# Kernel optimization log

Measured on AMD Instinct MI355X. Metric: run time of the kernel, lower is better.

## Reference

```python
import jax, jax.numpy as jnp
import numpy as np

B = 1024          # number of sessions (graphs)
D = 128           # emb_dim
NH = 4            # num_heads
VOCAB = 50000     # POI vocabulary
NDIST = 512       # distance buckets
MAX_LEN = 160     # max session length


def _lengths():
    # deterministic variable session lengths in [64, 160]
    return np.asarray(64 + (np.arange(B) % 97), dtype=np.int64)


def _layernorm(x, g, b, eps=1e-8):
    mu = x.mean(-1, keepdims=True)
    var = ((x - mu) ** 2).mean(-1, keepdims=True)
    return (x - mu) / jnp.sqrt(var + eps) * g + b


def setup_inputs() -> dict:
    key = jax.random.key(0)
    ks = jax.random.split(key, 16)
    lengths = _lengths()
    N = int(lengths.sum())
    # node -> (graph id, position within graph)
    batch_ids = np.repeat(np.arange(B), lengths)
    node_pos = np.concatenate([np.arange(l) for l in lengths])
    # consecutive (sequence) edges within each session
    starts = np.concatenate([[0], np.cumsum(lengths)[:-1]])
    src = np.concatenate([s + np.arange(l - 1) for s, l in zip(starts, lengths)])
    dst = src + 1
    edge_index = np.stack([src, dst]).astype(np.int64)
    E = edge_index.shape[1]
    s = 1.0 / np.sqrt(D)
    return {
        "POI_embs": jax.random.normal(ks[0], (VOCAB, D), jnp.float32) * 0.02,
        "delta_dis_embs": jax.random.normal(ks[1], (NDIST, D), jnp.float32) * 0.02,
        "att_W": jax.random.normal(ks[2], (D, D), jnp.float32) * s,
        "a_src": jax.random.normal(ks[3], (D,), jnp.float32) * 0.1,
        "a_dst": jax.random.normal(ks[4], (D,), jnp.float32) * 0.1,
        "in_proj_w": jax.random.normal(ks[5], (3 * D, D), jnp.float32) * s,
        "in_proj_b": jnp.zeros((3 * D,), jnp.float32),
        "out_proj_w": jax.random.normal(ks[6], (D, D), jnp.float32) * s,
        "out_proj_b": jnp.zeros((D,), jnp.float32),
        "ln1_g": jnp.ones((D,), jnp.float32), "ln1_b": jnp.zeros((D,), jnp.float32),
        "ln2_g": jnp.ones((D,), jnp.float32), "ln2_b": jnp.zeros((D,), jnp.float32),
        "ffn_w1": jax.random.normal(ks[7], (D, D), jnp.float32) * s,
        "ffn_b1": jnp.zeros((D,), jnp.float32),
        "ffn_w2": jax.random.normal(ks[8], (D, D), jnp.float32) * s,
        "ffn_b2": jnp.zeros((D,), jnp.float32),
        "sess_idx": jax.random.randint(ks[9], (N,), 0, VOCAB),
        "edge_dist": jax.random.randint(ks[10], (E,), 0, NDIST),
        "edge_index": jnp.asarray(edge_index),
        "batch_ids": jnp.asarray(batch_ids),
        "node_pos": jnp.asarray(node_pos),
        "lengths": jnp.asarray(lengths),
    }


def reference(POI_embs, delta_dis_embs, att_W, a_src, a_dst,
              in_proj_w, in_proj_b, out_proj_w, out_proj_b,
              ln1_g, ln1_b, ln2_g, ln2_b,
              ffn_w1, ffn_b1, ffn_w2, ffn_b2,
              sess_idx, edge_dist, edge_index, batch_ids, node_pos, lengths):
    N = sess_idx.shape[0]
    E = edge_index.shape[1]
    # ---- BiSeqGCN: gather -> attention logits -> scatter-softmax -> scatter-add
    x = POI_embs[sess_idx]                    # [N, D] node features
    edge_l = delta_dis_embs[edge_dist]        # [E, D] edge features
    src, dst = edge_index[0], edge_index[1]
    # bidirectional edges: forward (src->dst) then reversed (dst->src)
    j = jnp.concatenate([src, dst])           # message source  x_j
    i = jnp.concatenate([dst, src])           # message target  x_i
    x_i = x[i]                                # [2E, D]
    x_j = x[j]                                # [2E, D]
    fwd_coeff = (x_i[:E] + edge_l) @ att_W.T  # [E, D]
    bwd_coeff = x_i[E:] @ att_W.T             # [E, D]
    logits = jnp.concatenate([fwd_coeff @ a_src, bwd_coeff @ a_dst])  # [2E]
    # scatter-softmax over destination node (torch_geometric softmax, eps=1e-16)
    m = jax.ops.segment_max(logits, i, num_segments=N)
    e = jnp.exp(logits - m[i])
    ssum = jax.ops.segment_sum(e, i, num_segments=N)
    attn = e / (ssum[i] + 1e-16)
    H_u = jax.ops.segment_sum(x_j * attn[:, None], i, num_segments=N)  # [N, D]
    # ---- split/pad to [B, Lmax, D] + padding mask
    Bn = lengths.shape[0]
    pad = jnp.zeros((Bn, MAX_LEN, D), H_u.dtype).at[batch_ids, node_pos].set(H_u)
    mask = jnp.arange(MAX_LEN)[None, :] < lengths[:, None]  # [B, Lmax]
    # ---- MultiheadAttention (Q = LayerNorm(pad); K = V = pad)
    Q = _layernorm(pad, ln1_g, ln1_b)
    Wq, Wk, Wv = jnp.split(in_proj_w, 3, axis=0)
    bq, bk, bv = jnp.split(in_proj_b, 3)
    hd = D // NH
    q = (Q @ Wq.T + bq).reshape(Bn, MAX_LEN, NH, hd)
    k = (pad @ Wk.T + bk).reshape(Bn, MAX_LEN, NH, hd)
    v = (pad @ Wv.T + bv).reshape(Bn, MAX_LEN, NH, hd)
    scores = jnp.einsum('bqhd,bkhd->bhqk', q, k) / jnp.sqrt(jnp.asarray(hd, q.dtype))
    scores = jnp.where(mask[:, None, None, :], scores, -jnp.inf)
    w = jax.nn.softmax(scores, axis=-1)
    ctx = jnp.einsum('bhqk,bkhd->bqhd', w, v).reshape(Bn, MAX_LEN, D)
    out = ctx @ out_proj_w.T + out_proj_b
    out = out + Q
    out = _layernorm(out, ln2_g, ln2_b)
    # ---- PFFN (1x1 convs == per-token linears) with residual
    ffn = jax.nn.relu(out @ ffn_w1.T + ffn_b1) @ ffn_w2.T + ffn_b2
    out = out + ffn
    # ---- masked mean pool over valid positions
    mf = mask[..., None].astype(out.dtype)
    S_u = (out * mf).sum(axis=1) / lengths[:, None].astype(out.dtype)
    return S_u
```

## Files before the change

### kernel.cpp

```cpp
#include <hip/hip_runtime.h>
#include <float.h>


#define D 128
#define NHEAD 4
#define HD 32
#define MAXL 160
#define MAXNK 10
#define VP 168
#define WP 136

typedef __attribute__((ext_vector_type(8))) short short8;
typedef __attribute__((ext_vector_type(4))) float floatx4;

__device__ __forceinline__ float lo2f(unsigned u) {
    union { unsigned i; float f; } x; x.i = u << 16; return x.f;
}
__device__ __forceinline__ float hi2f(unsigned u) {
    union { unsigned i; float f; } x; x.i = u & 0xffff0000u; return x.f;
}
__device__ __forceinline__ unsigned pack2(float a, float b) {
    unsigned r;
    asm("v_cvt_pk_bf16_f32 %0, %1, %2" : "=v"(r) : "v"(a), "v"(b));
    return r;
}
__device__ __forceinline__ unsigned short f2bf(float f) {
    return (unsigned short)pack2(f, 0.f);
}
__device__ __forceinline__ unsigned short f2bfi(float f) {
    union { float f; unsigned i; } x; x.f = f;
    unsigned r = x.i + 0x7fffu + ((x.i >> 16) & 1u);
    return (unsigned short)(r >> 16);
}
__device__ __forceinline__ unsigned pack2i(float a, float b) {
    return (unsigned)f2bfi(a) | ((unsigned)f2bfi(b) << 16);
}
__device__ __forceinline__ float bf2f(unsigned short u) {
    union { unsigned i; float f; } x; x.i = (unsigned)u << 16; return x.f;
}

__launch_bounds__(128)
__global__ void prep1(const float* __restrict__ att_W, const float* __restrict__ a_src,
                      const float* __restrict__ a_dst, const float* __restrict__ in_proj_w,
                      const float* __restrict__ in_proj_b, const float* __restrict__ g1,
                      const float* __restrict__ b1, float* __restrict__ c_src,
                      float* __restrict__ c_dst, float* __restrict__ u, float* __restrict__ z) {
    int p = blockIdx.x;
    int q = threadIdx.x;
    __shared__ float red[4][2];
    float w  = att_W[q * D + p];
    float wq = in_proj_w[p * D + q];
    float s  = a_src[q] * w;
    float d  = a_dst[q] * w;
    float su = g1[q] * wq;
    float sz = b1[q] * wq;
    #pragma unroll
    for (int o = 32; o; o >>= 1) {
        s  += __shfl_down(s, o, 64);
        d  += __shfl_down(d, o, 64);
        su += __shfl_down(su, o, 64);
        sz += __shfl_down(sz, o, 64);
    }
    int wv = q >> 6;
    if ((q & 63) == 0) { red[0][wv] = s; red[1][wv] = d; red[2][wv] = su; red[3][wv] = sz; }
    __syncthreads();
    if (q == 0) {
        c_src[p] = red[0][0] + red[0][1];
        c_dst[p] = red[1][0] + red[1][1];
        u[p]     = red[2][0] + red[2][1];
        z[p]     = red[3][0] + red[3][1] + in_proj_b[p];
    }
}

__global__ void prep2(const float* __restrict__ delta, const float* __restrict__ c_src,
                      const float* __restrict__ in_proj_w, const float* __restrict__ out_proj_w,
                      const float* __restrict__ ffn_w1, const float* __restrict__ ffn_w2,
                      const float* __restrict__ ln1_g, float* __restrict__ tb,
                      unsigned short* __restrict__ wb) {
    int blk = blockIdx.x, t = threadIdx.x;
    if (blk < 128) {
        int b = blk * 4 + (t >> 6);
        int l = t & 63;
        const float* row = delta + (size_t)b * D;
        float s = row[l] * c_src[l] + row[l + 64] * c_src[l + 64];
        #pragma unroll
        for (int o = 32; o; o >>= 1) s += __shfl_down(s, o, 64);
        if (l == 0) tb[b] = s;
    } else {
        int idx = (blk - 128) * 256 + t;
        int m = idx >> 14;
        int within = idx & (D * D - 1);
        float v;
        if (m == 0) v = in_proj_w[within] * ln1_g[within & (D - 1)];
        else if (m == 1) v = in_proj_w[D * D + within];
        else if (m == 2) v = in_proj_w[2 * D * D + within];
        else if (m == 3) v = out_proj_w[within];
        else if (m == 4) v = ffn_w1[within];
        else v = ffn_w2[within];
        wb[idx] = f2bf(v);
    }
}

__launch_bounds__(256)
__global__ void gather_hu(const float* __restrict__ POI, const int* __restrict__ sess_idx,
                          const int* __restrict__ node_pos, const int* __restrict__ batch_ids,
                          const int* __restrict__ edge_dist, const int* __restrict__ lengths,
                          const float* __restrict__ c_src, const float* __restrict__ c_dst,
                          const float* __restrict__ tb, unsigned short* __restrict__ Hu,
                          float* __restrict__ muv, float* __restrict__ rinvv,
                          int* __restrict__ starts, int N) {
    __shared__ unsigned xs[10 * 64];
    __shared__ float s1s[10], s2s[10];
    int R0 = blockIdx.x * 8;
    int t = threadIdx.x;
    int hw = t >> 5, l32 = t & 31;
    float4 cs4 = *(const float4*)(c_src + l32 * 4);
    float4 cd4 = *(const float4*)(c_dst + l32 * 4);
    #pragma unroll
    for (int i = hw; i < 10; i += 8) {
        int n = R0 - 1 + i;
        if (n >= 0 && n < N) {
            int row = sess_idx[n];
            float4 v = *(const float4*)(POI + (size_t)row * D + l32 * 4);
            ((uint2*)(xs + i * 64))[l32] = make_uint2(pack2(v.x, v.y), pack2(v.z, v.w));
            if (i >= 1 && i <= 8) {
                float ps = v.x * cs4.x + v.y * cs4.y + v.z * cs4.z + v.w * cs4.w;
                float pd = v.x * cd4.x + v.y * cd4.y + v.z * cd4.z + v.w * cd4.w;
                #pragma unroll
                for (int o = 16; o; o >>= 1) {
                    ps += __shfl_down(ps, o, 64);
                    pd += __shfl_down(pd, o, 64);
                }
                if (l32 == 0) { s1s[i] = ps; s2s[i] = pd; }
            }
        }
    }
    __syncthreads();
    int j = hw;
    int n = R0 + j;
    if (n >= N) return;
    int g = batch_ids[n], pos = node_pos[n], L = lengths[g];
    bool hasF = pos > 0;
    bool hasB = pos < L - 1;
    float la = hasF ? (s1s[j + 1] + tb[edge_dist[n - 1 - g]]) : -FLT_MAX;
    float lb = hasB ? s2s[j + 1] : -FLT_MAX;
    float m = fmaxf(la, lb);
    float ea = hasF ? __expf(la - m) : 0.f;
    float eb = hasB ? __expf(lb - m) : 0.f;
    float inv = 1.f / (ea + eb + 1e-16f);
    float wa = ea * inv, wb = eb * inv;
    uint2 a = hasF ? ((const uint2*)(xs + j * 64))[l32] : make_uint2(0u, 0u);
    uint2 b = hasB ? ((const uint2*)(xs + (j + 2) * 64))[l32] : make_uint2(0u, 0u);
    float h0 = wa * lo2f(a.x) + wb * lo2f(b.x);
    float h1 = wa * hi2f(a.x) + wb * hi2f(b.x);
    float h2 = wa * lo2f(a.y) + wb * lo2f(b.y);
    float h3 = wa * hi2f(a.y) + wb * hi2f(b.y);
    ((uint2*)Hu)[(size_t)n * 32 + l32] = make_uint2(pack2(h0, h1), pack2(h2, h3));
    float s = h0 + h1 + h2 + h3;
    float ss = h0 * h0 + h1 * h1 + h2 * h2 + h3 * h3;
    #pragma unroll
    for (int o = 1; o < 32; o <<= 1) {
        s += __shfl_xor(s, o, 64);
        ss += __shfl_xor(ss, o, 64);
    }
    if (l32 == 0) {
        float mu = s * (1.f / D);
        float var = ss * (1.f / D) - mu * mu;
        muv[n] = mu;
        rinvv[n] = rsqrtf(var + 1e-8f);
        if (pos == 0) starts[g] = n;
    }
}

__launch_bounds__(256)
__global__ void qkv_split(const unsigned short* __restrict__ Hu, const unsigned short* __restrict__ wb,
                          const float* __restrict__ in_proj_b, const float* __restrict__ u,
                          const float* __restrict__ z, const float* __restrict__ muv,
                          const float* __restrict__ rinvv,
                          unsigned short* __restrict__ qo, unsigned short* __restrict__ ko,
                          unsigned short* __restrict__ vT, int M, int Npad) {
    __shared__ unsigned short Wl[128 * WP];
    int t = threadIdx.x;
    int wv = t >> 6, lane = t & 63;
    int quad = lane >> 4, l16 = lane & 15;
    int r0 = blockIdx.x * 128;
    int rbase = r0 + wv * 32;
    int p = blockIdx.y;
    const float ASCALE = 0.25504364148122793f;
    const unsigned short* W = wb + (p == 0 ? 1 : p == 1 ? 2 : 0) * (D * D);
    for (int i = t; i < 2048; i += 256) {
        int c = i >> 4, kc = (i & 15) * 8;
        *(uint4*)&Wl[c * WP + kc] = *(const uint4*)(W + c * 128 + kc);
    }
    short8 af[2][4];
    #pragma unroll
    for (int mt = 0; mt < 2; mt++) {
        int r = rbase + mt * 16 + l16;
        #pragma unroll
        for (int kk = 0; kk < 4; kk++) {
            if (r < M) af[mt][kk] = *(const short8*)(Hu + (size_t)r * D + kk * 32 + quad * 8);
            else af[mt][kk] = (short8){0, 0, 0, 0, 0, 0, 0, 0};
        }
    }
    __syncthreads();
    floatx4 acc[2][8];
    #pragma unroll
    for (int i = 0; i < 2; i++)
        #pragma unroll
        for (int j = 0; j < 8; j++) acc[i][j] = (floatx4){0.f, 0.f, 0.f, 0.f};
    #pragma unroll
    for (int kk = 0; kk < 4; kk++)
        #pragma unroll
        for (int nt = 0; nt < 8; nt++) {
            short8 bf = *(const short8*)&Wl[(nt * 16 + l16) * WP + kk * 32 + quad * 8];
            acc[0][nt] = __builtin_amdgcn_mfma_f32_16x16x32_bf16(af[0][kk], bf, acc[0][nt], 0, 0, 0);
            acc[1][nt] = __builtin_amdgcn_mfma_f32_16x16x32_bf16(af[1][kk], bf, acc[1][nt], 0, 0, 0);
        }
    __syncthreads();
    if (p == 1) {
        #pragma unroll
        for (int nt = 0; nt < 8; nt++) {
            int col = nt * 16 + l16;
            float bv = in_proj_b[2 * D + col];
            #pragma unroll
            for (int mt = 0; mt < 2; mt++)
                #pragma unroll
                for (int r = 0; r < 4; r += 2) {
                    int ln = wv * 32 + mt * 16 + quad * 4 + r;
                    float v0 = (r0 + ln     < M) ? acc[mt][nt][r]     + bv : 0.f;
                    float v1 = (r0 + ln + 1 < M) ? acc[mt][nt][r + 1] + bv : 0.f;
                    *(unsigned*)&Wl[col * WP + ln] = pack2(v0, v1);
                }
        }
    } else if (p == 0) {
        #pragma unroll
        for (int nt = 0; nt < 8; nt++) {
            int col = nt * 16 + l16;
            float bv = in_proj_b[D + col];
            #pragma unroll
            for (int mt = 0; mt < 2; mt++)
                #pragma unroll
                for (int r = 0; r < 4; r++)
                    Wl[(wv * 32 + mt * 16 + quad * 4 + r) * WP + col] =
                        f2bf(acc[mt][nt][r] + bv);
        }
    } else {
        float uc[8], zc[8];
        #pragma unroll
        for (int nt = 0; nt < 8; nt++) {
            uc[nt] = u[nt * 16 + l16];
            zc[nt] = z[nt * 16 + l16] * ASCALE;
        }
        #pragma unroll
        for (int mt = 0; mt < 2; mt++)
            #pragma unroll
            for (int r = 0; r < 4; r++) {
                int ln = wv * 32 + mt * 16 + quad * 4 + r;
                int grow = r0 + ln;
                float mr = grow < M ? muv[grow] : 0.f;
                float rr = (grow < M ? rinvv[grow] : 0.f) * ASCALE;
                #pragma unroll
                for (int nt = 0; nt < 8; nt++)
                    Wl[ln * WP + nt * 16 + l16] =
                        f2bf(rr * (acc[mt][nt][r] - mr * uc[nt]) + zc[nt]);
            }
    }
    __syncthreads();
    if (p == 1) {
        for (int i = t; i < 2048; i += 256) {
            int col = i >> 4, c8 = (i & 15) * 8;
            *(uint4*)(vT + (size_t)col * Npad + r0 + c8) = *(uint4*)&Wl[col * WP + c8];
        }
    } else {
        unsigned short* out = (p == 0) ? ko : qo;
        for (int i = t; i < 2048; i += 256) {
            int row = i >> 4, c8 = (i & 15) * 8;
            if (r0 + row < M)
                *(uint4*)(out + (size_t)(r0 + row) * D + c8) = *(uint4*)&Wl[row * WP + c8];
        }
    }
}

__launch_bounds__(128)
__global__ void attn9(const unsigned short* __restrict__ qb,
                      const unsigned short* __restrict__ kb,
                      const unsigned short* __restrict__ vT,
                      const int* __restrict__ starts, const int* __restrict__ lengths,
                      unsigned short* __restrict__ ctx, int Npad) {
    __shared__ unsigned short Vt[HD * VP];
    __shared__ unsigned short Pb[2 * 16 * VP];
    int g = blockIdx.x;
    if (gridDim.x == 1024) {
        int bid = blockIdx.x;
        if (bid < 430) { int r = 96 - bid / 10; g = r + 97 * (bid % 10); }
        else { int b2 = bid - 430; int r = 53 - b2 / 11; g = r + 97 * (b2 % 11); }
    }
    int h = blockIdx.y;
    int start = starts[g], L = lengths[g];
    int t = threadIdx.x;
    int wv = t >> 6, lane = t & 63;
    int l16 = lane & 15, quad = lane >> 4;
    int nk = (L + 15) >> 4;
    int nk2 = (L + 31) >> 5;
    unsigned short* Pw = Pb + wv * 16 * VP;
    if (nk & 1) {
        for (int i = lane; i < 128; i += 64) {
            int row = i >> 3, c = i & 7;
            ((unsigned*)(Pw + row * VP + nk * 16))[c] = 0u;
        }
    }
    int nch = nk2 * 4;
    for (int i = t; i < HD * nch; i += 128) {
        int r = i / nch, c = i - r * nch;
        *(uint4*)&Vt[r * VP + c * 8] =
            *(const uint4*)(vT + (size_t)(h * HD + r) * Npad + start + c * 8);
    }
    short8 kf[MAXNK];
    #pragma unroll
    for (int kt = 0; kt < MAXNK; kt++) {
        kf[kt] = (short8){0, 0, 0, 0, 0, 0, 0, 0};
        if (kt < nk) {
            int r = kt * 16 + l16;
            if (r < L) kf[kt] = *(const short8*)(kb + (size_t)(start + r) * D + h * HD + quad * 8);
        }
    }
    short8 qf[5];
    #pragma unroll
    for (int i = 0; i < 5; i++) {
        qf[i] = (short8){0, 0, 0, 0, 0, 0, 0, 0};
        int qt = wv + 2 * i;
        if (qt < nk) {
            int qrow = qt * 16 + l16;
            if (qrow < L)
                qf[i] = *(const short8*)(qb + (size_t)(start + qrow) * D + h * HD + quad * 8);
        }
    }
    __syncthreads();
    #pragma unroll
    for (int i = 0; i < 5; i++) {
        int qt = wv + 2 * i;
        if (qt >= nk) break;
        int q0 = qt * 16;
        floatx4 sacc[MAXNK];
        #pragma unroll
        for (int kt = 0; kt < MAXNK; kt++)
            if (kt < nk)
                sacc[kt] = __builtin_amdgcn_mfma_f32_16x16x32_bf16(
                    kf[kt], qf[i], (floatx4){0.f, 0.f, 0.f, 0.f}, 0, 0, 0);
        float lsum = 0.f;
        #pragma unroll
        for (int kt = 0; kt < MAXNK; kt++)
            if (kt < nk) {
                #pragma unroll
                for (int r = 0; r < 4; r++) {
                    int key = kt * 16 + quad * 4 + r;
                    float p = (key < L) ? __builtin_amdgcn_exp2f(sacc[kt][r]) : 0.f;
                    sacc[kt][r] = p;
                    lsum += p;
                }
                *(uint2*)&Pw[l16 * VP + kt * 16 + quad * 4] =
                    make_uint2(pack2i(sacc[kt][0], sacc[kt][1]),
                               pack2i(sacc[kt][2], sacc[kt][3]));
            }
        lsum += __shfl_xor(lsum, 16);
        lsum += __shfl_xor(lsum, 32);
        float inv = 1.f / lsum;
        #pragma unroll
        for (int nc = 0; nc < 2; nc++) {
            floatx4 oa = (floatx4){0.f, 0.f, 0.f, 0.f};
            floatx4 ob = (floatx4){0.f, 0.f, 0.f, 0.f};
            #pragma unroll
            for (int kc = 0; kc < 5; kc++)
                if (kc < nk2) {
                    short8 pf = *(const short8*)&Pw[l16 * VP + kc * 32 + quad * 8];
                    short8 vf = *(const short8*)&Vt[(nc * 16 + l16) * VP + kc * 32 + quad * 8];
                    if (kc & 1) ob = __builtin_amdgcn_mfma_f32_16x16x32_bf16(pf, vf, ob, 0, 0, 0);
                    else        oa = __builtin_amdgcn_mfma_f32_16x16x32_bf16(pf, vf, oa, 0, 0, 0);
                }
            #pragma unroll
            for (int r = 0; r < 4; r++) {
                int qr = q0 + quad * 4 + r;
                if (qr < L)
                    ctx[(size_t)(start + qr) * D + h * HD + nc * 16 + l16] =
                        f2bfi((oa[r] + ob[r]) * inv);
            }
        }
    }
}

__launch_bounds__(256)
__global__ void outproj_ln2(const unsigned short* __restrict__ ctx, const unsigned short* __restrict__ W,
                            const float* __restrict__ bo, const unsigned short* __restrict__ Hu,
                            const float* __restrict__ muv, const float* __restrict__ rinvv,
                            const float* __restrict__ g1, const float* __restrict__ b1,
                            const float* __restrict__ g2, const float* __restrict__ b2,
                            unsigned short* __restrict__ out, int M) {
    __shared__ unsigned short Wl[128 * WP];
    int t = threadIdx.x;
    int wv = t >> 6, lane = t & 63;
    int quad = lane >> 4, l16 = lane & 15;
    int r0 = blockIdx.x * 128;
    int rbase = r0 + wv * 32;
    for (int i = t; i < 2048; i += 256) {
        int c = i >> 4, kc = (i & 15) * 8;
        *(uint4*)&Wl[c * WP + kc] = *(const uint4*)(W + c * 128 + kc);
    }
    __syncthreads();
    floatx4 acc[2][8];
    #pragma unroll
    for (int i = 0; i < 2; i++)
        #pragma unroll
        for (int j = 0; j < 8; j++) acc[i][j] = (floatx4){0.f, 0.f, 0.f, 0.f};
    #pragma unroll
    for (int kk = 0; kk < 4; kk++) {
        short8 af[2];
        #pragma unroll
        for (int mt = 0; mt < 2; mt++) {
            int r = rbase + mt * 16 + l16;
            if (r < M) af[mt] = *(const short8*)(ctx + (size_t)r * D + kk * 32 + quad * 8);
            else af[mt] = (short8){0, 0, 0, 0, 0, 0, 0, 0};
        }
        #pragma unroll
        for (int nt = 0; nt < 8; nt++) {
            short8 bf = *(const short8*)&Wl[(nt * 16 + l16) * WP + kk * 32 + quad * 8];
            acc[0][nt] = __builtin_amdgcn_mfma_f32_16x16x32_bf16(af[0], bf, acc[0][nt], 0, 0, 0);
            acc[1][nt] = __builtin_amdgcn_mfma_f32_16x16x32_bf16(af[1], bf, acc[1][nt], 0, 0, 0);
        }
    }
    __syncthreads();
    for (int i = t; i < 2048; i += 256) {
        int row = i >> 4, c8 = (i & 15) * 8;
        uint4 hv = make_uint4(0u, 0u, 0u, 0u);
        if (r0 + row < M) hv = *(const uint4*)(Hu + (size_t)(r0 + row) * D + c8);
        *(uint4*)&Wl[row * WP + c8] = hv;
    }
    __syncthreads();
    float g1c[8], b1c[8], boc[8], g2c[8], b2c[8];
    #pragma unroll
    for (int nt = 0; nt < 8; nt++) {
        int col = nt * 16 + l16;
        g1c[nt] = g1[col]; b1c[nt] = b1[col]; boc[nt] = bo[col];
        g2c[nt] = g2[col]; b2c[nt] = b2[col];
    }
    #pragma unroll
    for (int mt = 0; mt < 2; mt++) {
        #pragma unroll
        for (int r = 0; r < 4; r++) {
            int lrow = wv * 32 + mt * 16 + quad * 4 + r;
            int grow = r0 + lrow;
            bool ok = grow < M;
            float mr = ok ? muv[grow] : 0.f;
            float rr = ok ? rinvv[grow] : 0.f;
            float vv[8];
            float s = 0.f, ss = 0.f;
            #pragma unroll
            for (int nt = 0; nt < 8; nt++) {
                float huv = bf2f(Wl[lrow * WP + nt * 16 + l16]);
                float qv = (huv - mr) * rr * g1c[nt] + b1c[nt];
                float v = acc[mt][nt][r] + boc[nt] + qv;
                vv[nt] = v;
                s += v; ss += v * v;
            }
            #pragma unroll
            for (int o = 1; o < 16; o <<= 1) {
                s += __shfl_xor(s, o, 64);
                ss += __shfl_xor(ss, o, 64);
            }
            float mu = s * (1.f / D);
            float var = ss * (1.f / D) - mu * mu;
            float rinv = rsqrtf(var + 1e-8f);
            #pragma unroll
            for (int nt = 0; nt < 8; nt++)
                Wl[lrow * WP + nt * 16 + l16] =
                    f2bf((vv[nt] - mu) * rinv * g2c[nt] + b2c[nt]);
        }
    }
    __syncthreads();
    for (int i = t; i < 2048; i += 256) {
        int row = i >> 4, c8 = (i & 15) * 8;
        if (r0 + row < M)
            *(uint4*)(out + (size_t)(r0 + row) * D + c8) = *(uint4*)&Wl[row * WP + c8];
    }
}

__launch_bounds__(256)
__global__ void ffn_fused(const unsigned short* __restrict__ out2, const unsigned short* __restrict__ W1,
                          const float* __restrict__ b1f, const unsigned short* __restrict__ W2,
                          const float* __restrict__ b2f, unsigned short* __restrict__ fin, int M) {
    __shared__ unsigned short Wl[128 * WP];
    int t = threadIdx.x;
    int wv = t >> 6, lane = t & 63;
    int quad = lane >> 4, l16 = lane & 15;
    int r0 = blockIdx.x * 128;
    int rbase = r0 + wv * 32;
    int lbase = wv * 32;
    for (int i = t; i < 2048; i += 256) {
        int c = i >> 4, kc = (i & 15) * 8;
        *(uint4*)&Wl[c * WP + kc] = *(const uint4*)(W1 + c * 128 + kc);
    }
    short8 af[2][4];
    #pragma unroll
    for (int mt = 0; mt < 2; mt++) {
        int r = rbase + mt * 16 + l16;
        #pragma unroll
        for (int kk = 0; kk < 4; kk++) {
            if (r < M) af[mt][kk] = *(const short8*)(out2 + (size_t)r * D + kk * 32 + quad * 8);
            else af[mt][kk] = (short8){0, 0, 0, 0, 0, 0, 0, 0};
        }
    }
    __syncthreads();
    floatx4 acc[2][8];
    #pragma unroll
    for (int i = 0; i < 2; i++)
        #pragma unroll
        for (int j = 0; j < 8; j++) acc[i][j] = (floatx4){0.f, 0.f, 0.f, 0.f};
    #pragma unroll
    for (int kk = 0; kk < 4; kk++)
        #pragma unroll
        for (int nt = 0; nt < 8; nt++) {
            short8 bf = *(const short8*)&Wl[(nt * 16 + l16) * WP + kk * 32 + quad * 8];
            acc[0][nt] = __builtin_amdgcn_mfma_f32_16x16x32_bf16(af[0][kk], bf, acc[0][nt], 0, 0, 0);
            acc[1][nt] = __builtin_amdgcn_mfma_f32_16x16x32_bf16(af[1][kk], bf, acc[1][nt], 0, 0, 0);
        }
    __syncthreads();
    #pragma unroll
    for (int nt = 0; nt < 8; nt++) {
        int col = nt * 16 + l16;
        float bv = b1f[col];
        #pragma unroll
        for (int mt = 0; mt < 2; mt++)
            #pragma unroll
            for (int r = 0; r < 4; r++)
                Wl[(lbase + mt * 16 + quad * 4 + r) * WP + col] =
                    f2bf(fmaxf(acc[mt][nt][r] + bv, 0.f));
    }
    __syncthreads();
    short8 af2[2][4];
    #pragma unroll
    for (int mt = 0; mt < 2; mt++)
        #pragma unroll
        for (int kk = 0; kk < 4; kk++)
            af2[mt][kk] = *(const short8*)&Wl[(lbase + mt * 16 + l16) * WP + kk * 32 + quad * 8];
    __syncthreads();
    for (int i = t; i < 2048; i += 256) {
        int c = i >> 4, kc = (i & 15) * 8;
        *(uint4*)&Wl[c * WP + kc] = *(const uint4*)(W2 + c * 128 + kc);
    }
    __syncthreads();
    #pragma unroll
    for (int i = 0; i < 2; i++)
        #pragma unroll
        for (int j = 0; j < 8; j++) acc[i][j] = (floatx4){0.f, 0.f, 0.f, 0.f};
    #pragma unroll
    for (int kk = 0; kk < 4; kk++)
        #pragma unroll
        for (int nt = 0; nt < 8; nt++) {
            short8 bf = *(const short8*)&Wl[(nt * 16 + l16) * WP + kk * 32 + quad * 8];
            acc[0][nt] = __builtin_amdgcn_mfma_f32_16x16x32_bf16(af2[0][kk], bf, acc[0][nt], 0, 0, 0);
            acc[1][nt] = __builtin_amdgcn_mfma_f32_16x16x32_bf16(af2[1][kk], bf, acc[1][nt], 0, 0, 0);
        }
    __syncthreads();
    #pragma unroll
    for (int nt = 0; nt < 8; nt++) {
        int col = nt * 16 + l16;
        float bv = b2f[col];
        #pragma unroll
        for (int mt = 0; mt < 2; mt++)
            #pragma unroll
            for (int r = 0; r < 4; r++)
                Wl[(lbase + mt * 16 + quad * 4 + r) * WP + col] = f2bf(acc[mt][nt][r] + bv);
    }
    __syncthreads();
    for (int i = t; i < 2048; i += 256) {
        int row = i >> 4, c8 = (i & 15) * 8;
        int grow = r0 + row;
        if (grow < M) {
            uint4 a = *(uint4*)&Wl[row * WP + c8];
            uint4 b = *(const uint4*)(out2 + (size_t)grow * D + c8);
            uint4 o;
            o.x = pack2(lo2f(a.x) + lo2f(b.x), hi2f(a.x) + hi2f(b.x));
            o.y = pack2(lo2f(a.y) + lo2f(b.y), hi2f(a.y) + hi2f(b.y));
            o.z = pack2(lo2f(a.z) + lo2f(b.z), hi2f(a.z) + hi2f(b.z));
            o.w = pack2(lo2f(a.w) + lo2f(b.w), hi2f(a.w) + hi2f(b.w));
            *(uint4*)(fin + (size_t)grow * D + c8) = o;
        }
    }
}

__launch_bounds__(512)
__global__ void pool_k(const unsigned short* __restrict__ fin, const int* __restrict__ starts,
                       const int* __restrict__ lengths, float* __restrict__ out) {
    __shared__ float ps[4][128];
    int g = blockIdx.x;
    int t = threadIdx.x;
    int d = t & 127, qt = t >> 7;
    int start = starts[g], L = lengths[g];
    int qlen = (L + 3) >> 2;
    int p0 = qt * qlen;
    int p1 = min(L, p0 + qlen);
    float s0 = 0.f, s1 = 0.f, s2 = 0.f, s3 = 0.f;
    int p = p0;
    for (; p + 4 <= p1; p += 4) {
        s0 += bf2f(fin[(size_t)(start + p) * D + d]);
        s1 += bf2f(fin[(size_t)(start + p + 1) * D + d]);
        s2 += bf2f(fin[(size_t)(start + p + 2) * D + d]);
        s3 += bf2f(fin[(size_t)(start + p + 3) * D + d]);
    }
    for (; p < p1; p++) s0 += bf2f(fin[(size_t)(start + p) * D + d]);
    ps[qt][d] = (s0 + s1) + (s2 + s3);
    __syncthreads();
    if (qt == 0)
        out[(size_t)g * D + d] =
            ((ps[0][d] + ps[1][d]) + (ps[2][d] + ps[3][d])) / (float)L;
}

extern "C" void kernel_launch(void* const* d_in, const int* in_sizes, int n_in,
                              void* d_out, int out_size, void* d_ws, size_t ws_size,
                              hipStream_t stream) {
    const float* POI        = (const float*)d_in[0];
    const float* delta      = (const float*)d_in[1];
    const float* att_W      = (const float*)d_in[2];
    const float* a_src      = (const float*)d_in[3];
    const float* a_dst      = (const float*)d_in[4];
    const float* in_proj_w  = (const float*)d_in[5];
    const float* in_proj_b  = (const float*)d_in[6];
    const float* out_proj_w = (const float*)d_in[7];
    const float* out_proj_b = (const float*)d_in[8];
    const float* ln1_g      = (const float*)d_in[9];
    const float* ln1_b      = (const float*)d_in[10];
    const float* ln2_g      = (const float*)d_in[11];
    const float* ln2_b      = (const float*)d_in[12];
    const float* ffn_w1     = (const float*)d_in[13];
    const float* ffn_b1     = (const float*)d_in[14];
    const float* ffn_w2     = (const float*)d_in[15];
    const float* ffn_b2     = (const float*)d_in[16];
    const int* sess_idx     = (const int*)d_in[17];
    const int* edge_dist    = (const int*)d_in[18];
    const int* batch_ids    = (const int*)d_in[20];
    const int* node_pos     = (const int*)d_in[21];
    const int* lengths      = (const int*)d_in[22];

    int N = in_sizes[17];
    int B = in_sizes[22];
    int gb = (N + 127) / 128;
    int Npad = gb * 128;

    char* base = (char*)d_ws;
    size_t off = 0;
    auto alloc = [&](size_t bytes) { size_t c = off; off = (off + bytes + 255) & ~(size_t)255; return c; };
    size_t o_csrc  = alloc(D * 4);
    size_t o_cdst  = alloc(D * 4);
    size_t o_t     = alloc(512 * 4);
    size_t o_start = alloc((size_t)B * 4);
    size_t o_mu    = alloc((size_t)N * 4);
    size_t o_ri    = alloc((size_t)N * 4);
    size_t o_u     = alloc(D * 4);
    size_t o_z     = alloc(D * 4);
    size_t o_wb    = alloc(6 * D * D * 2);
    size_t nb      = (size_t)Npad * D * 2;
    size_t o_A = alloc(nb);
    size_t o_B = alloc(nb);
    size_t o_C = alloc(nb);
    size_t o_D = alloc(nb);
    if (ws_size < off) return;

    float* c_src = (float*)(base + o_csrc);
    float* c_dst = (float*)(base + o_cdst);
    float* tb    = (float*)(base + o_t);
    int*   starts = (int*)(base + o_start);
    float* muv   = (float*)(base + o_mu);
    float* rinvv = (float*)(base + o_ri);
    float* u     = (float*)(base + o_u);
    float* z     = (float*)(base + o_z);
    unsigned short* wb = (unsigned short*)(base + o_wb);
    unsigned short* bufA = (unsigned short*)(base + o_A);
    unsigned short* bufB = (unsigned short*)(base + o_B);
    unsigned short* bufC = (unsigned short*)(base + o_C);
    unsigned short* bufD = (unsigned short*)(base + o_D);

    prep1<<<128, 128, 0, stream>>>(att_W, a_src, a_dst, in_proj_w, in_proj_b,
                                   ln1_g, ln1_b, c_src, c_dst, u, z);
    prep2<<<512, 256, 0, stream>>>(delta, c_src, in_proj_w, out_proj_w,
                                   ffn_w1, ffn_w2, ln1_g, tb, wb);
    gather_hu<<<(N + 7) / 8, 256, 0, stream>>>(POI, sess_idx, node_pos, batch_ids,
                                               edge_dist, lengths, c_src, c_dst, tb,
                                               bufB, muv, rinvv, starts, N);

    qkv_split<<<dim3(gb, 3), 256, 0, stream>>>(bufB, wb, in_proj_b, u, z, muv, rinvv,
                                               bufC, bufD, bufA, N, Npad);

    attn9<<<dim3(B, NHEAD), 128, 0, stream>>>(bufC, bufD, bufA, starts, lengths, bufC, Npad);

    outproj_ln2<<<gb, 256, 0, stream>>>(bufC, wb + 3 * D * D, out_proj_b, bufB, muv, rinvv,
                                        ln1_g, ln1_b, ln2_g, ln2_b, bufD, N);
    ffn_fused<<<gb, 256, 0, stream>>>(bufD, wb + 4 * D * D, ffn_b1, wb + 5 * D * D, ffn_b2,
                                      bufA, N);
    pool_k<<<B, 512, 0, stream>>>(bufA, starts, lengths, (float*)d_out);
}
```

Baseline: 301.1 us.

## Fuse Q/K/V projections into one kernel and double-buffer attention P tiles

The QKV projection no longer launches three grid slices, one per projection. Each block now loads its activation fragments once and runs the K, V and Q GEMMs in sequence, reloading the weight tile into shared memory between them. This cuts activation reloads and block count, but the projections now run serially inside a block, which lowers parallelism and adds barriers. The attention kernel also gives each wave two P buffers, alternating per query tile, so writes for the next tile do not conflict with reads of the previous one. That doubles the shared memory for P.

```diff
diff --git a/kernel.cpp b/kernel.cpp
--- a/kernel.cpp
+++ b/kernel.cpp
@@ -173,7 +173,7 @@
 }
 
 __launch_bounds__(256)
-__global__ void qkv_split(const unsigned short* __restrict__ Hu, const unsigned short* __restrict__ wb,
+__global__ void qkv_fused(const unsigned short* __restrict__ Hu, const unsigned short* __restrict__ wb,
                           const float* __restrict__ in_proj_b, const float* __restrict__ u,
                           const float* __restrict__ z, const float* __restrict__ muv,
                           const float* __restrict__ rinvv,
@@ -185,13 +185,8 @@
     int quad = lane >> 4, l16 = lane & 15;
     int r0 = blockIdx.x * 128;
     int rbase = r0 + wv * 32;
-    int p = blockIdx.y;
     const float ASCALE = 0.25504364148122793f;
-    const unsigned short* W = wb + (p == 0 ? 1 : p == 1 ? 2 : 0) * (D * D);
-    for (int i = t; i < 2048; i += 256) {
-        int c = i >> 4, kc = (i & 15) * 8;
-        *(uint4*)&Wl[c * WP + kc] = *(const uint4*)(W + c * 128 + kc);
-    }
+
     short8 af[2][4];
     #pragma unroll
     for (int mt = 0; mt < 2; mt++) {
@@ -202,8 +197,13 @@
             else af[mt][kk] = (short8){0, 0, 0, 0, 0, 0, 0, 0};
         }
     }
-    __syncthreads();
     floatx4 acc[2][8];
+
+    for (int i = t; i < 2048; i += 256) {
+        int c = i >> 4, kc = (i & 15) * 8;
+        *(uint4*)&Wl[c * WP + kc] = *(const uint4*)(wb + 1 * D * D + c * 128 + kc);
+    }
+    __syncthreads();
     #pragma unroll
     for (int i = 0; i < 2; i++)
         #pragma unroll
@@ -217,34 +217,83 @@
             acc[1][nt] = __builtin_amdgcn_mfma_f32_16x16x32_bf16(af[1][kk], bf, acc[1][nt], 0, 0, 0);
         }
     __syncthreads();
-    if (p == 1) {
+    #pragma unroll
+    for (int nt = 0; nt < 8; nt++) {
+        int col = nt * 16 + l16;
+        float bv = in_proj_b[D + col];
+        #pragma unroll
+        for (int mt = 0; mt < 2; mt++)
+            #pragma unroll
+            for (int r = 0; r < 4; r++)
+                Wl[(wv * 32 + mt * 16 + quad * 4 + r) * WP + col] =
+                    f2bf(acc[mt][nt][r] + bv);
+    }
+    __syncthreads();
+    for (int i = t; i < 2048; i += 256) {
+        int row = i >> 4, c8 = (i & 15) * 8;
+        if (r0 + row < M)
+            *(uint4*)(ko + (size_t)(r0 + row) * D + c8) = *(uint4*)&Wl[row * WP + c8];
+    }
+    __syncthreads();
+
+    for (int i = t; i < 2048; i += 256) {
+        int c = i >> 4, kc = (i & 15) * 8;
+        *(uint4*)&Wl[c * WP + kc] = *(const uint4*)(wb + 2 * D * D + c * 128 + kc);
+    }
+    __syncthreads();
+    #pragma unroll
+    for (int i = 0; i < 2; i++)
+        #pragma unroll
+        for (int j = 0; j < 8; j++) acc[i][j] = (floatx4){0.f, 0.f, 0.f, 0.f};
+    #pragma unroll
+    for (int kk = 0; kk < 4; kk++)
         #pragma unroll
         for (int nt = 0; nt < 8; nt++) {
-            int col = nt * 16 + l16;
-            float bv = in_proj_b[2 * D + col];
-            #pragma unroll
-            for (int mt = 0; mt < 2; mt++)
-                #pragma unroll
-                for (int r = 0; r < 4; r += 2) {
-                    int ln = wv * 32 + mt * 16 + quad * 4 + r;
-                    float v0 = (r0 + ln     < M) ? acc[mt][nt][r]     + bv : 0.f;
-                    float v1 = (r0 + ln + 1 < M) ? acc[mt][nt][r + 1] + bv : 0.f;
-                    *(unsigned*)&Wl[col * WP + ln] = pack2(v0, v1);
-                }
-        }
-    } else if (p == 0) {
+            short8 bf = *(const short8*)&Wl[(nt * 16 + l16) * WP + kk * 32 + quad * 8];
+            acc[0][nt] = __builtin_amdgcn_mfma_f32_16x16x32_bf16(af[0][kk], bf, acc[0][nt], 0, 0, 0);
+            acc[1][nt] = __builtin_amdgcn_mfma_f32_16x16x32_bf16(af[1][kk], bf, acc[1][nt], 0, 0, 0);
+        }
+    __syncthreads();
+    #pragma unroll
+    for (int nt = 0; nt < 8; nt++) {
+        int col = nt * 16 + l16;
+        float bv = in_proj_b[2 * D + col];
+        #pragma unroll
+        for (int mt = 0; mt < 2; mt++)
+            #pragma unroll
+            for (int r = 0; r < 4; r += 2) {
+                int ln = wv * 32 + mt * 16 + quad * 4 + r;
+                float v0 = (r0 + ln     < M) ? acc[mt][nt][r]     + bv : 0.f;
+                float v1 = (r0 + ln + 1 < M) ? acc[mt][nt][r + 1] + bv : 0.f;
+                *(unsigned*)&Wl[col * WP + ln] = pack2(v0, v1);
+            }
+    }
+    __syncthreads();
+    for (int i = t; i < 2048; i += 256) {
+        int col = i >> 4, c8 = (i & 15) * 8;
+        *(uint4*)(vT + (size_t)col * Npad + r0 + c8) = *(uint4*)&Wl[col * WP + c8];
+    }
+    __syncthreads();
+
+    for (int i = t; i < 2048; i += 256) {
+        int c = i >> 4, kc = (i & 15) * 8;
+        *(uint4*)&Wl[c * WP + kc] = *(const uint4*)(wb + 0 * D * D + c * 128 + kc);
+    }
+    __syncthreads();
+    #pragma unroll
+    for (int i = 0; i < 2; i++)
+        #pragma unroll
+        for (int j = 0; j < 8; j++) acc[i][j] = (floatx4){0.f, 0.f, 0.f, 0.f};
+    #pragma unroll
+    for (int kk = 0; kk < 4; kk++)
         #pragma unroll
         for (int nt = 0; nt < 8; nt++) {
-            int col = nt * 16 + l16;
-            float bv = in_proj_b[D + col];
-            #pragma unroll
-            for (int mt = 0; mt < 2; mt++)
-                #pragma unroll
-                for (int r = 0; r < 4; r++)
-                    Wl[(wv * 32 + mt * 16 + quad * 4 + r) * WP + col] =
-                        f2bf(acc[mt][nt][r] + bv);
-        }
-    } else {
+            short8 bf = *(const short8*)&Wl[(nt * 16 + l16) * WP + kk * 32 + quad * 8];
+            acc[0][nt] = __builtin_amdgcn_mfma_f32_16x16x32_bf16(af[0][kk], bf, acc[0][nt], 0, 0, 0);
+            acc[1][nt] = __builtin_amdgcn_mfma_f32_16x16x32_bf16(af[1][kk], bf, acc[1][nt], 0, 0, 0);
+        }
+    __syncthreads();
+    {
         float uc[8], zc[8];
         #pragma unroll
         for (int nt = 0; nt < 8; nt++) {
@@ -266,18 +315,10 @@
             }
     }
     __syncthreads();
-    if (p == 1) {
-        for (int i = t; i < 2048; i += 256) {
-            int col = i >> 4, c8 = (i & 15) * 8;
-            *(uint4*)(vT + (size_t)col * Npad + r0 + c8) = *(uint4*)&Wl[col * WP + c8];
-        }
-    } else {
-        unsigned short* out = (p == 0) ? ko : qo;
-        for (int i = t; i < 2048; i += 256) {
-            int row = i >> 4, c8 = (i & 15) * 8;
-            if (r0 + row < M)
-                *(uint4*)(out + (size_t)(r0 + row) * D + c8) = *(uint4*)&Wl[row * WP + c8];
-        }
+    for (int i = t; i < 2048; i += 256) {
+        int row = i >> 4, c8 = (i & 15) * 8;
+        if (r0 + row < M)
+            *(uint4*)(qo + (size_t)(r0 + row) * D + c8) = *(uint4*)&Wl[row * WP + c8];
     }
 }
 
@@ -288,7 +329,7 @@
                       const int* __restrict__ starts, const int* __restrict__ lengths,
                       unsigned short* __restrict__ ctx, int Npad) {
     __shared__ unsigned short Vt[HD * VP];
-    __shared__ unsigned short Pb[2 * 16 * VP];
+    __shared__ unsigned short Pb[4 * 16 * VP];
     int g = blockIdx.x;
     if (gridDim.x == 1024) {
         int bid = blockIdx.x;
@@ -302,11 +343,12 @@
     int l16 = lane & 15, quad = lane >> 4;
     int nk = (L + 15) >> 4;
     int nk2 = (L + 31) >> 5;
-    unsigned short* Pw = Pb + wv * 16 * VP;
     if (nk & 1) {
-        for (int i = lane; i < 128; i += 64) {
-            int row = i >> 3, c = i & 7;
-            ((unsigned*)(Pw + row * VP + nk * 16))[c] = 0u;
+        for (int i = lane; i < 256; i += 64) {
+            int buf = i >> 7;
+            int j = i & 127;
+            int row = j >> 3, c = j & 7;
+            ((unsigned*)(Pb + (wv * 2 + buf) * 16 * VP + row * VP + nk * 16))[c] = 0u;
         }
     }
     int nch = nk2 * 4;
@@ -341,6 +383,7 @@
         int qt = wv + 2 * i;
         if (qt >= nk) break;
         int q0 = qt * 16;
+        unsigned short* Pw = Pb + (wv * 2 + (i & 1)) * 16 * VP;
         floatx4 sacc[MAXNK];
         #pragma unroll
         for (int kt = 0; kt < MAXNK; kt++)
@@ -686,8 +729,8 @@
                                                edge_dist, lengths, c_src, c_dst, tb,
                                                bufB, muv, rinvv, starts, N);
 
-    qkv_split<<<dim3(gb, 3), 256, 0, stream>>>(bufB, wb, in_proj_b, u, z, muv, rinvv,
-                                               bufC, bufD, bufA, N, Npad);
+    qkv_fused<<<gb, 256, 0, stream>>>(bufB, wb, in_proj_b, u, z, muv, rinvv,
+                                      bufC, bufD, bufA, N, Npad);
 
     attn9<<<dim3(B, NHEAD), 128, 0, stream>>>(bufC, bufD, bufA, starts, lengths, bufC, Npad);
 
```

New measurement: 318.5 us. 1.06x slower.

## Fuse out-projection, LN2, FFN and mean-pool into one tail kernel with atomics

Applied to the files above, without the earlier changes.

Merges the out-projection + LayerNorm2 kernel, the FFN kernel and the pooling kernel into one per-128-row kernel. The LN2 output stays in LDS and feeds the FFN directly. The residual is folded into pooling by pooling the LN2 output and the FFN output separately and adding both into the output with per-graph atomicAdds. This removes the intermediate bf16 global round trips (out2 and fin) and two launches, at the cost of a memset, float atomics whose accumulation order is nondeterministic, and slightly different rounding because the residual is no longer summed in bf16.

```diff
diff --git a/kernel.cpp b/kernel.cpp
--- a/kernel.cpp
+++ b/kernel.cpp
@@ -389,127 +389,140 @@
 }
 
 __launch_bounds__(256)
-__global__ void outproj_ln2(const unsigned short* __restrict__ ctx, const unsigned short* __restrict__ W,
-                            const float* __restrict__ bo, const unsigned short* __restrict__ Hu,
-                            const float* __restrict__ muv, const float* __restrict__ rinvv,
-                            const float* __restrict__ g1, const float* __restrict__ b1,
-                            const float* __restrict__ g2, const float* __restrict__ b2,
-                            unsigned short* __restrict__ out, int M) {
+__global__ void tail_fused(const unsigned short* __restrict__ ctx,
+                           const unsigned short* __restrict__ Wo,
+                           const float* __restrict__ bo,
+                           const unsigned short* __restrict__ Hu,
+                           const float* __restrict__ muv, const float* __restrict__ rinvv,
+                           const float* __restrict__ g1, const float* __restrict__ b1,
+                           const float* __restrict__ g2, const float* __restrict__ b2,
+                           const unsigned short* __restrict__ W1,
+                           const float* __restrict__ b1f,
+                           const unsigned short* __restrict__ W2,
+                           const float* __restrict__ b2f,
+                           const int* __restrict__ batch_ids,
+                           const int* __restrict__ lengths,
+                           float* __restrict__ out, int M) {
     __shared__ unsigned short Wl[128 * WP];
-    int t = threadIdx.x;
-    int wv = t >> 6, lane = t & 63;
-    int quad = lane >> 4, l16 = lane & 15;
-    int r0 = blockIdx.x * 128;
-    int rbase = r0 + wv * 32;
-    for (int i = t; i < 2048; i += 256) {
-        int c = i >> 4, kc = (i & 15) * 8;
-        *(uint4*)&Wl[c * WP + kc] = *(const uint4*)(W + c * 128 + kc);
-    }
-    __syncthreads();
-    floatx4 acc[2][8];
-    #pragma unroll
-    for (int i = 0; i < 2; i++)
-        #pragma unroll
-        for (int j = 0; j < 8; j++) acc[i][j] = (floatx4){0.f, 0.f, 0.f, 0.f};
-    #pragma unroll
-    for (int kk = 0; kk < 4; kk++) {
-        short8 af[2];
-        #pragma unroll
-        for (int mt = 0; mt < 2; mt++) {
-            int r = rbase + mt * 16 + l16;
-            if (r < M) af[mt] = *(const short8*)(ctx + (size_t)r * D + kk * 32 + quad * 8);
-            else af[mt] = (short8){0, 0, 0, 0, 0, 0, 0, 0};
-        }
-        #pragma unroll
-        for (int nt = 0; nt < 8; nt++) {
-            short8 bf = *(const short8*)&Wl[(nt * 16 + l16) * WP + kk * 32 + quad * 8];
-            acc[0][nt] = __builtin_amdgcn_mfma_f32_16x16x32_bf16(af[0], bf, acc[0][nt], 0, 0, 0);
-            acc[1][nt] = __builtin_amdgcn_mfma_f32_16x16x32_bf16(af[1], bf, acc[1][nt], 0, 0, 0);
-        }
-    }
-    __syncthreads();
-    for (int i = t; i < 2048; i += 256) {
-        int row = i >> 4, c8 = (i & 15) * 8;
-        uint4 hv = make_uint4(0u, 0u, 0u, 0u);
-        if (r0 + row < M) hv = *(const uint4*)(Hu + (size_t)(r0 + row) * D + c8);
-        *(uint4*)&Wl[row * WP + c8] = hv;
-    }
-    __syncthreads();
-    float g1c[8], b1c[8], boc[8], g2c[8], b2c[8];
-    #pragma unroll
-    for (int nt = 0; nt < 8; nt++) {
-        int col = nt * 16 + l16;
-        g1c[nt] = g1[col]; b1c[nt] = b1[col]; boc[nt] = bo[col];
-        g2c[nt] = g2[col]; b2c[nt] = b2[col];
-    }
-    #pragma unroll
-    for (int mt = 0; mt < 2; mt++) {
-        #pragma unroll
-        for (int r = 0; r < 4; r++) {
-            int lrow = wv * 32 + mt * 16 + quad * 4 + r;
-            int grow = r0 + lrow;
-            bool ok = grow < M;
-            float mr = ok ? muv[grow] : 0.f;
-            float rr = ok ? rinvv[grow] : 0.f;
-            float vv[8];
-            float s = 0.f, ss = 0.f;
-            #pragma unroll
-            for (int nt = 0; nt < 8; nt++) {
-                float huv = bf2f(Wl[lrow * WP + nt * 16 + l16]);
-                float qv = (huv - mr) * rr * g1c[nt] + b1c[nt];
-                float v = acc[mt][nt][r] + boc[nt] + qv;
-                vv[nt] = v;
-                s += v; ss += v * v;
-            }
-            #pragma unroll
-            for (int o = 1; o < 16; o <<= 1) {
-                s += __shfl_xor(s, o, 64);
-                ss += __shfl_xor(ss, o, 64);
-            }
-            float mu = s * (1.f / D);
-            float var = ss * (1.f / D) - mu * mu;
-            float rinv = rsqrtf(var + 1e-8f);
-            #pragma unroll
-            for (int nt = 0; nt < 8; nt++)
-                Wl[lrow * WP + nt * 16 + l16] =
-                    f2bf((vv[nt] - mu) * rinv * g2c[nt] + b2c[nt]);
-        }
-    }
-    __syncthreads();
-    for (int i = t; i < 2048; i += 256) {
-        int row = i >> 4, c8 = (i & 15) * 8;
-        if (r0 + row < M)
-            *(uint4*)(out + (size_t)(r0 + row) * D + c8) = *(uint4*)&Wl[row * WP + c8];
-    }
-}
-
-__launch_bounds__(256)
-__global__ void ffn_fused(const unsigned short* __restrict__ out2, const unsigned short* __restrict__ W1,
-                          const float* __restrict__ b1f, const unsigned short* __restrict__ W2,
-                          const float* __restrict__ b2f, unsigned short* __restrict__ fin, int M) {
-    __shared__ unsigned short Wl[128 * WP];
+    __shared__ int gids[128];
     int t = threadIdx.x;
     int wv = t >> 6, lane = t & 63;
     int quad = lane >> 4, l16 = lane & 15;
     int r0 = blockIdx.x * 128;
     int rbase = r0 + wv * 32;
     int lbase = wv * 32;
+    int rmax = min(128, M - r0);
+
+    for (int i = t; i < 2048; i += 256) {
+        int c = i >> 4, kc = (i & 15) * 8;
+        *(uint4*)&Wl[c * WP + kc] = *(const uint4*)(Wo + c * 128 + kc);
+    }
+    if (t < 128) gids[t] = (r0 + t < M) ? batch_ids[r0 + t] : -1;
+    short8 af[2][4];
+    #pragma unroll
+    for (int mt = 0; mt < 2; mt++) {
+        int r = rbase + mt * 16 + l16;
+        #pragma unroll
+        for (int kk = 0; kk < 4; kk++) {
+            if (r < M) af[mt][kk] = *(const short8*)(ctx + (size_t)r * D + kk * 32 + quad * 8);
+            else af[mt][kk] = (short8){0, 0, 0, 0, 0, 0, 0, 0};
+        }
+    }
+    __syncthreads();
+    floatx4 acc[2][8];
+    #pragma unroll
+    for (int i = 0; i < 2; i++)
+        #pragma unroll
+        for (int j = 0; j < 8; j++) acc[i][j] = (floatx4){0.f, 0.f, 0.f, 0.f};
+    #pragma unroll
+    for (int kk = 0; kk < 4; kk++)
+        #pragma unroll
+        for (int nt = 0; nt < 8; nt++) {
+            short8 bf = *(const short8*)&Wl[(nt * 16 + l16) * WP + kk * 32 + quad * 8];
+            acc[0][nt] = __builtin_amdgcn_mfma_f32_16x16x32_bf16(af[0][kk], bf, acc[0][nt], 0, 0, 0);
+            acc[1][nt] = __builtin_amdgcn_mfma_f32_16x16x32_bf16(af[1][kk], bf, acc[1][nt], 0, 0, 0);
+        }
+    __syncthreads();
+
+    for (int i = t; i < 2048; i += 256) {
+        int row = i >> 4, c8 = (i & 15) * 8;
+        uint4 hv = make_uint4(0u, 0u, 0u, 0u);
+        if (r0 + row < M) hv = *(const uint4*)(Hu + (size_t)(r0 + row) * D + c8);
+        *(uint4*)&Wl[row * WP + c8] = hv;
+    }
+    __syncthreads();
+    {
+        float g1c[8], b1c[8], boc[8], g2c[8], b2c[8];
+        #pragma unroll
+        for (int nt = 0; nt < 8; nt++) {
+            int col = nt * 16 + l16;
+            g1c[nt] = g1[col]; b1c[nt] = b1[col]; boc[nt] = bo[col];
+            g2c[nt] = g2[col]; b2c[nt] = b2[col];
+        }
+        #pragma unroll
+        for (int mt = 0; mt < 2; mt++) {
+            #pragma unroll
+            for (int r = 0; r < 4; r++) {
+                int lrow = wv * 32 + mt * 16 + quad * 4 + r;
+                int grow = r0 + lrow;
+                bool ok = grow < M;
+                float mr = ok ? muv[grow] : 0.f;
+                float rr = ok ? rinvv[grow] : 0.f;
+                float vv[8];
+                float s = 0.f, ss = 0.f;
+                #pragma unroll
+                for (int nt = 0; nt < 8; nt++) {
+                    float huv = bf2f(Wl[lrow * WP + nt * 16 + l16]);
+                    float qv = (huv - mr) * rr * g1c[nt] + b1c[nt];
+                    float v = acc[mt][nt][r] + boc[nt] + qv;
+                    vv[nt] = v;
+                    s += v; ss += v * v;
+                }
+                #pragma unroll
+                for (int o = 1; o < 16; o <<= 1) {
+                    s += __shfl_xor(s, o, 64);
+                    ss += __shfl_xor(ss, o, 64);
+                }
+                float mu = s * (1.f / D);
+                float var = ss * (1.f / D) - mu * mu;
+                float rinv = rsqrtf(var + 1e-8f);
+                #pragma unroll
+                for (int nt = 0; nt < 8; nt++)
+                    Wl[lrow * WP + nt * 16 + l16] =
+                        f2bf((vv[nt] - mu) * rinv * g2c[nt] + b2c[nt]);
+            }
+        }
+    }
+    __syncthreads();
+
+    short8 af2[2][4];
+    #pragma unroll
+    for (int mt = 0; mt < 2; mt++)
+        #pragma unroll
+        for (int kk = 0; kk < 4; kk++)
+            af2[mt][kk] = *(const short8*)&Wl[(lbase + mt * 16 + l16) * WP + kk * 32 + quad * 8];
+    {
+        int d = t & 127, half = t >> 7;
+        int rlo = half * 64, rhi = min(rlo + 64, rmax);
+        float sum = 0.f;
+        int cur = (rlo < rmax) ? gids[rlo] : -1;
+        for (int row = rlo; row < rhi; row++) {
+            int g = gids[row];
+            if (g != cur) {
+                atomicAdd(out + (size_t)cur * D + d, sum / (float)lengths[cur]);
+                sum = 0.f; cur = g;
+            }
+            sum += bf2f(Wl[row * WP + d]);
+        }
+        if (cur >= 0) atomicAdd(out + (size_t)cur * D + d, sum / (float)lengths[cur]);
+    }
+    __syncthreads();
+
     for (int i = t; i < 2048; i += 256) {
         int c = i >> 4, kc = (i & 15) * 8;
         *(uint4*)&Wl[c * WP + kc] = *(const uint4*)(W1 + c * 128 + kc);
     }
-    short8 af[2][4];
-    #pragma unroll
-    for (int mt = 0; mt < 2; mt++) {
-        int r = rbase + mt * 16 + l16;
-        #pragma unroll
-        for (int kk = 0; kk < 4; kk++) {
-            if (r < M) af[mt][kk] = *(const short8*)(out2 + (size_t)r * D + kk * 32 + quad * 8);
-            else af[mt][kk] = (short8){0, 0, 0, 0, 0, 0, 0, 0};
-        }
-    }
-    __syncthreads();
-    floatx4 acc[2][8];
+    __syncthreads();
     #pragma unroll
     for (int i = 0; i < 2; i++)
         #pragma unroll
@@ -519,8 +532,8 @@
         #pragma unroll
         for (int nt = 0; nt < 8; nt++) {
             short8 bf = *(const short8*)&Wl[(nt * 16 + l16) * WP + kk * 32 + quad * 8];
-            acc[0][nt] = __builtin_amdgcn_mfma_f32_16x16x32_bf16(af[0][kk], bf, acc[0][nt], 0, 0, 0);
-            acc[1][nt] = __builtin_amdgcn_mfma_f32_16x16x32_bf16(af[1][kk], bf, acc[1][nt], 0, 0, 0);
+            acc[0][nt] = __builtin_amdgcn_mfma_f32_16x16x32_bf16(af2[0][kk], bf, acc[0][nt], 0, 0, 0);
+            acc[1][nt] = __builtin_amdgcn_mfma_f32_16x16x32_bf16(af2[1][kk], bf, acc[1][nt], 0, 0, 0);
         }
     __syncthreads();
     #pragma unroll
@@ -535,13 +548,14 @@
                     f2bf(fmaxf(acc[mt][nt][r] + bv, 0.f));
     }
     __syncthreads();
-    short8 af2[2][4];
+    short8 af3[2][4];
     #pragma unroll
     for (int mt = 0; mt < 2; mt++)
         #pragma unroll
         for (int kk = 0; kk < 4; kk++)
-            af2[mt][kk] = *(const short8*)&Wl[(lbase + mt * 16 + l16) * WP + kk * 32 + quad * 8];
-    __syncthreads();
+            af3[mt][kk] = *(const short8*)&Wl[(lbase + mt * 16 + l16) * WP + kk * 32 + quad * 8];
+    __syncthreads();
+
     for (int i = t; i < 2048; i += 256) {
         int c = i >> 4, kc = (i & 15) * 8;
         *(uint4*)&Wl[c * WP + kc] = *(const uint4*)(W2 + c * 128 + kc);
@@ -556,8 +570,8 @@
         #pragma unroll
         for (int nt = 0; nt < 8; nt++) {
             short8 bf = *(const short8*)&Wl[(nt * 16 + l16) * WP + kk * 32 + quad * 8];
-            acc[0][nt] = __builtin_amdgcn_mfma_f32_16x16x32_bf16(af2[0][kk], bf, acc[0][nt], 0, 0, 0);
-            acc[1][nt] = __builtin_amdgcn_mfma_f32_16x16x32_bf16(af2[1][kk], bf, acc[1][nt], 0, 0, 0);
+            acc[0][nt] = __builtin_amdgcn_mfma_f32_16x16x32_bf16(af3[0][kk], bf, acc[0][nt], 0, 0, 0);
+            acc[1][nt] = __builtin_amdgcn_mfma_f32_16x16x32_bf16(af3[1][kk], bf, acc[1][nt], 0, 0, 0);
         }
     __syncthreads();
     #pragma unroll
@@ -571,47 +585,21 @@
                 Wl[(lbase + mt * 16 + quad * 4 + r) * WP + col] = f2bf(acc[mt][nt][r] + bv);
     }
     __syncthreads();
-    for (int i = t; i < 2048; i += 256) {
-        int row = i >> 4, c8 = (i & 15) * 8;
-        int grow = r0 + row;
-        if (grow < M) {
-            uint4 a = *(uint4*)&Wl[row * WP + c8];
-            uint4 b = *(const uint4*)(out2 + (size_t)grow * D + c8);
-            uint4 o;
-            o.x = pack2(lo2f(a.x) + lo2f(b.x), hi2f(a.x) + hi2f(b.x));
-            o.y = pack2(lo2f(a.y) + lo2f(b.y), hi2f(a.y) + hi2f(b.y));
-            o.z = pack2(lo2f(a.z) + lo2f(b.z), hi2f(a.z) + hi2f(b.z));
-            o.w = pack2(lo2f(a.w) + lo2f(b.w), hi2f(a.w) + hi2f(b.w));
-            *(uint4*)(fin + (size_t)grow * D + c8) = o;
-        }
-    }
-}
-
-__launch_bounds__(512)
-__global__ void pool_k(const unsigned short* __restrict__ fin, const int* __restrict__ starts,
-                       const int* __restrict__ lengths, float* __restrict__ out) {
-    __shared__ float ps[4][128];
-    int g = blockIdx.x;
-    int t = threadIdx.x;
-    int d = t & 127, qt = t >> 7;
-    int start = starts[g], L = lengths[g];
-    int qlen = (L + 3) >> 2;
-    int p0 = qt * qlen;
-    int p1 = min(L, p0 + qlen);
-    float s0 = 0.f, s1 = 0.f, s2 = 0.f, s3 = 0.f;
-    int p = p0;
-    for (; p + 4 <= p1; p += 4) {
-        s0 += bf2f(fin[(size_t)(start + p) * D + d]);
-        s1 += bf2f(fin[(size_t)(start + p + 1) * D + d]);
-        s2 += bf2f(fin[(size_t)(start + p + 2) * D + d]);
-        s3 += bf2f(fin[(size_t)(start + p + 3) * D + d]);
-    }
-    for (; p < p1; p++) s0 += bf2f(fin[(size_t)(start + p) * D + d]);
-    ps[qt][d] = (s0 + s1) + (s2 + s3);
-    __syncthreads();
-    if (qt == 0)
-        out[(size_t)g * D + d] =
-            ((ps[0][d] + ps[1][d]) + (ps[2][d] + ps[3][d])) / (float)L;
+    {
+        int d = t & 127, half = t >> 7;
+        int rlo = half * 64, rhi = min(rlo + 64, rmax);
+        float sum = 0.f;
+        int cur = (rlo < rmax) ? gids[rlo] : -1;
+        for (int row = rlo; row < rhi; row++) {
+            int g = gids[row];
+            if (g != cur) {
+                atomicAdd(out + (size_t)cur * D + d, sum / (float)lengths[cur]);
+                sum = 0.f; cur = g;
+            }
+            sum += bf2f(Wl[row * WP + d]);
+        }
+        if (cur >= 0) atomicAdd(out + (size_t)cur * D + d, sum / (float)lengths[cur]);
+    }
 }
 
 extern "C" void kernel_launch(void* const* d_in, const int* in_sizes, int n_in,
@@ -677,7 +665,9 @@
     unsigned short* bufB = (unsigned short*)(base + o_B);
     unsigned short* bufC = (unsigned short*)(base + o_C);
     unsigned short* bufD = (unsigned short*)(base + o_D);
-
+    (void)bufD;
+
+    hipMemsetAsync(d_out, 0, (size_t)B * D * 4, stream);
     prep1<<<128, 128, 0, stream>>>(att_W, a_src, a_dst, in_proj_w, in_proj_b,
                                    ln1_g, ln1_b, c_src, c_dst, u, z);
     prep2<<<512, 256, 0, stream>>>(delta, c_src, in_proj_w, out_proj_w,
@@ -691,9 +681,8 @@
 
     attn9<<<dim3(B, NHEAD), 128, 0, stream>>>(bufC, bufD, bufA, starts, lengths, bufC, Npad);
 
-    outproj_ln2<<<gb, 256, 0, stream>>>(bufC, wb + 3 * D * D, out_proj_b, bufB, muv, rinvv,
-                                        ln1_g, ln1_b, ln2_g, ln2_b, bufD, N);
-    ffn_fused<<<gb, 256, 0, stream>>>(bufD, wb + 4 * D * D, ffn_b1, wb + 5 * D * D, ffn_b2,
-                                      bufA, N);
-    pool_k<<<B, 512, 0, stream>>>(bufA, starts, lengths, (float*)d_out);
-}
+    tail_fused<<<gb, 256, 0, stream>>>(bufC, wb + 3 * D * D, out_proj_b, bufB, muv, rinvv,
+                                       ln1_g, ln1_b, ln2_g, ln2_b,
+                                       wb + 4 * D * D, ffn_b1, wb + 5 * D * D, ffn_b2,
+                                       batch_ids, lengths, (float*)d_out, N);
+}
```

New measurement: 301.6 us. Within noise of the previous version (+0.2%).
